# Performance work log

Hardware: AMD Instinct MI355X
Metric: run time of the kernel (lower is better)

## Reference

```python
import jax, jax.numpy as jnp
import numpy as np

E = 1024
H = 16
D = E // H  # head dim 64
B = 2
S = 2048


def setup_inputs() -> dict:
    key = jax.random.key(0)
    k1, k2, k3, k4, k5 = jax.random.split(key, 5)
    scale = 1.0 / np.sqrt(E)
    return {
        "x": jax.random.normal(k1, (B, S, E), dtype=jnp.float32),
        "W_in": jax.random.normal(k2, (E, 3 * E), dtype=jnp.float32) * scale,
        "b_in": jnp.zeros((3 * E,), dtype=jnp.float32),
        "W_out": jax.random.normal(k3, (E, E), dtype=jnp.float32) * scale,
        "b_out": jnp.zeros((E,), dtype=jnp.float32),
        "causal_mask": 1,
    }


def reference(x, W_in, b_in, W_out, b_out, causal_mask):
    b, s, e = x.shape
    qkv = x @ W_in + b_in                      # [B,S,3E]
    q, k, v = jnp.split(qkv, 3, axis=-1)
    # [B,S,E] -> [B,H,S,D]
    q = q.reshape(b, s, H, D).transpose(0, 2, 1, 3)
    k = k.reshape(b, s, H, D).transpose(0, 2, 1, 3)
    v = v.reshape(b, s, H, D).transpose(0, 2, 1, 3)
    scores = jnp.einsum("bhqd,bhkd->bhqk", q, k)
    if causal_mask:
        # mask applied before scaling in the original; -inf is scale-invariant
        mask = jnp.triu(jnp.ones((s, s), dtype=bool), k=1)
        scores = jnp.where(mask, -jnp.inf, scores)
    scores = scores / np.sqrt(D)
    weight = jax.nn.softmax(scores, axis=-1)
    out = jnp.einsum("bhqk,bhkd->bhqd", weight, v)   # [B,H,S,D]
    out = out.transpose(0, 2, 1, 3).reshape(b, s, e)
    return out @ W_out + b_out
```

## Files before the change

### kernel.cpp

```cpp
#include <hip/hip_runtime.h>
#include <hip/hip_bf16.h>
#include <cmath>

typedef __bf16 bf16;
typedef __attribute__((ext_vector_type(8))) __bf16 bf16x8;
typedef __attribute__((ext_vector_type(4))) __bf16 bf16x4;
typedef __attribute__((ext_vector_type(4))) float f32x4;
typedef __attribute__((ext_vector_type(16))) float f32x16;
typedef unsigned int u32;

constexpr int S  = 2048;
constexpr int E  = 1024;
constexpr int H  = 16;
constexpr int D  = 64;
constexpr int B  = 2;
constexpr int M  = B * S;
constexpr int N3 = 3 * E;
constexpr int NROWS = B * H * S;

static __device__ __forceinline__ void gload16(const void* g, void* l) {
  __builtin_amdgcn_global_load_lds((const __attribute__((address_space(1))) void*)g,
                                   (__attribute__((address_space(3))) void*)l, 16, 0, 0);
}

static __device__ __forceinline__ u32 pack2(float a, float b) {
  union { bf16 h[2]; u32 u; } r;
  r.h[0] = (bf16)a; r.h[1] = (bf16)b;
  return r.u;
}
typedef union { u32 w[4]; bf16x8 v; } FU;

__global__ void k_cvt(const float* __restrict__ in, bf16* __restrict__ out) {
  const int i = (blockIdx.x * blockDim.x + threadIdx.x) * 4;
  const float4 v = *(const float4*)(in + i);
  bf16x4 o = { (bf16)v.x, (bf16)v.y, (bf16)v.z, (bf16)v.w };
  *(bf16x4*)(out + i) = o;
}

__global__ void k_transpose_cvt(const float* __restrict__ in, bf16* __restrict__ out,
                                int R, int C) {
  __shared__ float t[32][33];
  const int c0 = blockIdx.x * 32, r0 = blockIdx.y * 32;
  const int tx = threadIdx.x, ty = threadIdx.y;
  #pragma unroll
  for (int j = 0; j < 32; j += 8)
    t[ty + j][tx] = in[(size_t)(r0 + ty + j) * C + c0 + tx];
  __syncthreads();
  #pragma unroll
  for (int j = 0; j < 32; j += 8)
    out[(size_t)(c0 + ty + j) * R + r0 + tx] = (bf16)t[tx][ty + j];
}

template<int EPI>
__global__ __launch_bounds__(256) void k_gemm(
    const bf16* __restrict__ A, const bf16* __restrict__ Bt,
    const float* __restrict__ bias, float* __restrict__ outF,
    bf16* __restrict__ oQ, bf16* __restrict__ oK, bf16* __restrict__ oV,
    int Kdim, int Nn)
{
  __shared__ __align__(16) char smem[65536];
  const int tid = threadIdx.x;
  const int lane = tid & 63, w = tid >> 6;
  const int lane15 = lane & 15, quad = lane >> 4;
  const int wm = w >> 1, wn = w & 1;

  const int nbx = Nn >> 7;
  const int nwg = gridDim.x;
  const int bid = blockIdx.x;
  const int swz = (bid & 7) * (nwg >> 3) + (bid >> 3);
  const int bn0 = (swz % nbx) * 128;
  const int bm0 = (swz / nbx) * 128;

  const int so0 = w * 1024 + lane * 16;
  int srow[4], slk[4];
  #pragma unroll
  for (int p = 0; p < 4; ++p) {
    const int o = p * 4096 + so0;
    const int row = o >> 7, cbyte = o & 127;
    srow[p] = row;
    slk[p] = (cbyte ^ ((row & 7) << 4)) >> 1;
  }

  f32x4 acc[4][4] = {};
  const int nkt = Kdim >> 6;

  #pragma unroll
  for (int p = 0; p < 4; ++p) {
    gload16(A  + (size_t)(bm0 + srow[p]) * Kdim + slk[p], smem +         p * 4096 + w * 1024);
    gload16(Bt + (size_t)(bn0 + srow[p]) * Kdim + slk[p], smem + 32768 + p * 4096 + w * 1024);
  }

  #pragma unroll 1
  for (int kt = 0; kt < nkt; ++kt) {
    const int cur = kt & 1;
    __builtin_amdgcn_s_barrier();
    if (kt + 1 < nkt) {
      const int k0 = (kt + 1) << 6;
      const int nb = (cur ^ 1) * 16384;
      #pragma unroll
      for (int p = 0; p < 4; ++p) {
        gload16(A  + (size_t)(bm0 + srow[p]) * Kdim + k0 + slk[p],
                smem + nb +         p * 4096 + w * 1024);
        gload16(Bt + (size_t)(bn0 + srow[p]) * Kdim + k0 + slk[p],
                smem + nb + 32768 + p * 4096 + w * 1024);
      }
      asm volatile("s_waitcnt vmcnt(8)" ::: "memory");
    } else {
      asm volatile("s_waitcnt vmcnt(0)" ::: "memory");
    }
    __builtin_amdgcn_s_barrier();

    const char* cA = smem + cur * 16384;
    const char* cB = smem + 32768 + cur * 16384;
    #pragma unroll
    for (int kk = 0; kk < 2; ++kk) {
      bf16x8 af[4], bfr[4];
      #pragma unroll
      for (int f = 0; f < 4; ++f) {
        const int ra = wm * 64 + f * 16 + lane15;
        af[f] = *(const bf16x8*)(cA + ra * 128 +
                 ((kk * 64 + (quad << 4)) ^ ((ra & 7) << 4)));
        const int rb = wn * 64 + f * 16 + lane15;
        bfr[f] = *(const bf16x8*)(cB + rb * 128 +
                 ((kk * 64 + (quad << 4)) ^ ((rb & 7) << 4)));
      }
      #pragma unroll
      for (int i = 0; i < 4; ++i)
        #pragma unroll
        for (int j = 0; j < 4; ++j)
          acc[i][j] = __builtin_amdgcn_mfma_f32_16x16x32_bf16(af[i], bfr[j], acc[i][j], 0, 0, 0);
    }
  }

  if constexpr (EPI == 1) {
    #pragma unroll
    for (int i = 0; i < 4; ++i)
      #pragma unroll
      for (int j = 0; j < 4; ++j) {
        const int n = bn0 + wn * 64 + j * 16 + lane15;
        const float bv = bias[n];
        #pragma unroll
        for (int r = 0; r < 4; ++r) {
          const int m = bm0 + wm * 64 + i * 16 + quad * 4 + r;
          outF[(size_t)m * E + n] = acc[i][j][r] + bv;
        }
      }
  } else {
    const int which = bn0 >> 10;
    const int b  = bm0 >> 11;
    const int s0 = bm0 & (S - 1);
    const int cn0 = bn0 & (E - 1);
    if (which < 2) {
      bf16* dst = (which == 0) ? oQ : oK;
      __builtin_amdgcn_s_barrier();
      char* lC = smem;
      #pragma unroll
      for (int j = 0; j < 4; ++j) {
        const int n_loc = wn * 64 + j * 16 + lane15;
        const float bv = bias[bn0 + n_loc];
        #pragma unroll
        for (int i = 0; i < 4; ++i)
          #pragma unroll
          for (int r = 0; r < 4; ++r) {
            const int m_loc = wm * 64 + i * 16 + quad * 4 + r;
            *(bf16*)(lC + m_loc * 256 + ((n_loc * 2) ^ ((m_loc & 7) << 4))) =
                (bf16)(acc[i][j][r] + bv);
          }
      }
      __builtin_amdgcn_s_barrier();
      const int h0 = cn0 >> 6;
      #pragma unroll
      for (int it = 0; it < 8; ++it) {
        const int cch = w * 64 + it * 8 + (lane >> 3);
        const int m_loc = cch >> 1, hh = cch & 1, piece = lane & 7;
        const bf16x8 vv = *(const bf16x8*)(lC + m_loc * 256 +
                          ((hh * 128 + piece * 16) ^ ((m_loc & 7) << 4)));
        *(bf16x8*)(dst + ((size_t)(b * H + h0 + hh) * S + s0 + m_loc) * D + piece * 8) = vv;
      }
    } else {
      #pragma unroll
      for (int j = 0; j < 4; ++j) {
        const int n_loc = wn * 64 + j * 16 + lane15;
        const int cn = cn0 + n_loc;
        const int h = cn >> 6, d = cn & 63;
        const float bv = bias[bn0 + n_loc];
        bf16* base = oV + ((size_t)(b * H + h) * D + d) * S + s0 + wm * 64;
        #pragma unroll
        for (int i = 0; i < 4; ++i) {
          bf16x4 pk = { (bf16)(acc[i][j][0] + bv), (bf16)(acc[i][j][1] + bv),
                        (bf16)(acc[i][j][2] + bv), (bf16)(acc[i][j][3] + bv) };
          *(bf16x4*)(base + i * 16 + quad * 4) = pk;
        }
      }
    }
  }
}

__global__ __launch_bounds__(256, 2) void k_attn(
    const bf16* __restrict__ Qb, const bf16* __restrict__ Kb, const bf16* __restrict__ Vt,
    bf16* __restrict__ pO0, bf16* __restrict__ pO1,
    float* __restrict__ pM, float* __restrict__ pL, const int* __restrict__ cmask)
{
  __shared__ __align__(16) char lK[2][64 * 128];
  __shared__ __align__(16) char lV[2][64 * 128];
  __shared__ __align__(16) float corr_lds[4][32];
  __shared__ __align__(16) float lrow_lds[4][32];

  const int tid = threadIdx.x, lane = tid & 63, w = tid >> 6;
  const int h = lane >> 5, q31 = lane & 31;
  const int bh = blockIdx.x;
  const int jb = blockIdx.y;
  const int causal = cmask[0];
  const float S2 = 0.18033688011112042f;

  const bf16* Qh = Qb + (size_t)bh * S * D;
  const bf16* Kh = Kb + (size_t)bh * S * D;
  const bf16* Vh = Vt + (size_t)bh * D * S;

  const int so0 = w * 1024 + lane * 16;
  int srow[2], slk[2];
  #pragma unroll
  for (int p = 0; p < 2; ++p) {
    const int o = p * 4096 + so0;
    const int row = o >> 7, cbv = o & 127;
    srow[p] = row;
    slk[p] = (cbv ^ ((row & 7) << 4)) >> 1;
  }
  const int swz = (q31 & 7) << 4;

  #pragma unroll 1
  for (int pidx = 0; pidx < 2; ++pidx) {
    const int c  = pidx ? (15 - jb) : jb;
    const int t0 = causal ? (pidx ? (c + 1) : 0) : (pidx ? 16 : 0);
    const int t1 = causal ? (pidx ? (2 * c + 2) : (c + 1)) : (pidx ? 32 : 16);
    const int q0w = c * 128 + 32 * w;
    const int qg  = q0w + q31;

    __builtin_amdgcn_s_barrier();

    bf16x8 qf[4];
    #pragma unroll
    for (int ds = 0; ds < 4; ++ds)
      qf[ds] = *(const bf16x8*)(Qh + (size_t)qg * D + 16 * ds + 8 * h);

    #pragma unroll
    for (int p = 0; p < 2; ++p) {
      gload16(Kh + (size_t)(t0 * 64 + srow[p]) * D + slk[p], lK[0] + p * 4096 + so0);
      gload16(Vh + (size_t)srow[p] * S + t0 * 64 + slk[p],   lV[0] + p * 4096 + so0);
    }

    f32x16 o0 = {}, o1 = {};
    float mrun = -INFINITY, lr = 0.f;

    #pragma unroll 1
    for (int t = t0; t < t1; ++t) {
      const int cb = (t - t0) & 1;
      __builtin_amdgcn_s_barrier();
      if (t + 1 < t1) {
        const int kb = (t + 1) * 64;
        #pragma unroll
        for (int p = 0; p < 2; ++p) {
          gload16(Kh + (size_t)(kb + srow[p]) * D + slk[p], lK[cb ^ 1] + p * 4096 + so0);
          gload16(Vh + (size_t)srow[p] * S + kb + slk[p],   lV[cb ^ 1] + p * 4096 + so0);
        }
        asm volatile("s_waitcnt vmcnt(4)" ::: "memory");
      } else {
        asm volatile("s_waitcnt vmcnt(0)" ::: "memory");
      }
      __builtin_amdgcn_s_barrier();

      const bool active = !causal || (64 * t <= q0w + 31);
      if (active) {
        f32x16 s0v = {}, s1v = {};
        __builtin_amdgcn_s_setprio(1);
        #pragma unroll
        for (int ds = 0; ds < 4; ++ds) {
          const int col = (32 * ds + 16 * h) ^ swz;
          const bf16x8 kf0 = *(const bf16x8*)(lK[cb] + q31 * 128 + col);
          const bf16x8 kf1 = *(const bf16x8*)(lK[cb] + (32 + q31) * 128 + col);
          s0v = __builtin_amdgcn_mfma_f32_32x32x16_bf16(kf0, qf[ds], s0v, 0, 0, 0);
          s1v = __builtin_amdgcn_mfma_f32_32x32x16_bf16(kf1, qf[ds], s1v, 0, 0, 0);
        }
        __builtin_amdgcn_s_setprio(0);

        if (causal && (64 * t + 63 > q0w)) {
          #pragma unroll
          for (int r = 0; r < 16; ++r) {
            const int kg = 64 * t + (r & 3) + 8 * (r >> 2) + 4 * h;
            if (kg > qg)      s0v[r] = -INFINITY;
            if (kg + 32 > qg) s1v[r] = -INFINITY;
          }
        }

        float a8[8];
        #pragma unroll
        for (int i = 0; i < 8; ++i)
          a8[i] = fmaxf(fmaxf(s0v[i], s0v[i + 8]), fmaxf(s1v[i], s1v[i + 8]));
        float tmax = fmaxf(fmaxf(fmaxf(a8[0], a8[1]), fmaxf(a8[2], a8[3])),
                           fmaxf(fmaxf(a8[4], a8[5]), fmaxf(a8[6], a8[7])));
        tmax = fmaxf(tmax, __shfl_xor(tmax, 32, 64));

        const bool nogrow = __all(tmax <= mrun);
        const float mnew = nogrow ? mrun : fmaxf(mrun, tmax);
        float corrf = 1.f;
        if (!nogrow) {
          corrf = __builtin_amdgcn_exp2f((mrun - mnew) * S2);
          corr_lds[w][q31] = corrf;
        }
        const float msc = mnew * S2;

        #pragma unroll
        for (int r = 0; r < 16; ++r) {
          s0v[r] = __builtin_amdgcn_exp2f(__builtin_fmaf(s0v[r], S2, -msc));
          s1v[r] = __builtin_amdgcn_exp2f(__builtin_fmaf(s1v[r], S2, -msc));
        }

        float b8[8];
        #pragma unroll
        for (int i = 0; i < 8; ++i)
          b8[i] = (s0v[i] + s0v[i + 8]) + (s1v[i] + s1v[i + 8]);
        float psum = ((b8[0] + b8[1]) + (b8[2] + b8[3])) + ((b8[4] + b8[5]) + (b8[6] + b8[7]));
        psum += __shfl_xor(psum, 32, 64);
        lr = lr * corrf + psum;
        mrun = mnew;

        u32 pk[8][2];
        #pragma unroll
        for (int jj = 0; jj < 4; ++jj) {
          pk[jj][0]     = pack2(s0v[4 * jj],     s0v[4 * jj + 1]);
          pk[jj][1]     = pack2(s0v[4 * jj + 2], s0v[4 * jj + 3]);
          pk[jj + 4][0] = pack2(s1v[4 * jj],     s1v[4 * jj + 1]);
          pk[jj + 4][1] = pack2(s1v[4 * jj + 2], s1v[4 * jj + 3]);
        }

        if (!nogrow) {
          #pragma unroll
          for (int j = 0; j < 4; ++j) {
            const f32x4 cv = *(const f32x4*)&corr_lds[w][8 * j + 4 * h];
            #pragma unroll
            for (int sr = 0; sr < 4; ++sr) {
              o0[4 * j + sr] *= cv[sr];
              o1[4 * j + sr] *= cv[sr];
            }
          }
        }

        __builtin_amdgcn_s_setprio(1);
        #pragma unroll
        for (int ks = 0; ks < 4; ++ks) {
          u32 a0 = pk[2 * ks][0], b0 = pk[2 * ks + 1][0];
          u32 a1 = pk[2 * ks][1], b1 = pk[2 * ks + 1][1];
          asm volatile("v_permlane32_swap_b32 %0, %1" : "+v"(a0), "+v"(b0));
          asm volatile("v_permlane32_swap_b32 %0, %1" : "+v"(a1), "+v"(b1));
          FU f; f.w[0] = a0; f.w[1] = a1; f.w[2] = b0; f.w[3] = b1;
          const int col = (32 * ks + 16 * h) ^ swz;
          const bf16x8 vf0 = *(const bf16x8*)(lV[cb] + q31 * 128 + col);
          const bf16x8 vf1 = *(const bf16x8*)(lV[cb] + (32 + q31) * 128 + col);
          o0 = __builtin_amdgcn_mfma_f32_32x32x16_bf16(f.v, vf0, o0, 0, 0, 0);
          o1 = __builtin_amdgcn_mfma_f32_32x32x16_bf16(f.v, vf1, o1, 0, 0, 0);
        }
        __builtin_amdgcn_s_setprio(0);
      }
    }

    if (h == 0) {
      pM[(size_t)pidx * NROWS + bh * S + qg] = mrun;
      pL[(size_t)pidx * NROWS + bh * S + qg] = lr;
    }
    lrow_lds[w][q31] = lr;
    bf16* po = pidx ? pO1 : pO0;
    #pragma unroll
    for (int j = 0; j < 4; ++j) {
      const f32x4 lv = *(const f32x4*)&lrow_lds[w][8 * j + 4 * h];
      #pragma unroll
      for (int sr = 0; sr < 4; ++sr) {
        const int r = 4 * j + sr;
        const float inv = lv[sr] > 0.f ? 1.0f / lv[sr] : 0.f;
        const int qrow = q0w + (r & 3) + 8 * (r >> 2) + 4 * h;
        bf16* dst = po + ((size_t)(bh * S + qrow)) * D;
        dst[q31]      = (bf16)(o0[r] * inv);
        dst[32 + q31] = (bf16)(o1[r] * inv);
      }
    }
  }
}

__global__ __launch_bounds__(256) void k_combine(
    const bf16* __restrict__ pO0, const bf16* __restrict__ pO1,
    const float* __restrict__ pM, const float* __restrict__ pL,
    bf16* __restrict__ AO)
{
  const float S2 = 0.18033688011112042f;
  const int idx = blockIdx.x * 256 + threadIdx.x;
  const int row = idx >> 3, d0 = (idx & 7) * 8;
  const float mA = pM[row], mB = pM[NROWS + row];
  const float lA = pL[row], lB = pL[NROWS + row];
  const float m = fmaxf(mA, mB);
  const float wA = lA > 0.f ? lA * __builtin_amdgcn_exp2f((mA - m) * S2) : 0.f;
  const float wB = lB > 0.f ? lB * __builtin_amdgcn_exp2f((mB - m) * S2) : 0.f;
  const float inv = 1.0f / (wA + wB);
  const bf16x8 a = *(const bf16x8*)(pO0 + (size_t)row * D + d0);
  const bf16x8 b = *(const bf16x8*)(pO1 + (size_t)row * D + d0);
  bf16x8 o;
  #pragma unroll
  for (int i = 0; i < 8; ++i)
    o[i] = (bf16)((wA * (float)a[i] + wB * (float)b[i]) * inv);
  const int bb = row >> 15, hh = (row >> 11) & 15, s = row & 2047;
  *(bf16x8*)(AO + ((size_t)(bb * S + s)) * E + hh * D + d0) = o;
}

extern "C" void kernel_launch(void* const* d_in, const int* in_sizes, int n_in,
                              void* d_out, int out_size, void* d_ws, size_t ws_size,
                              hipStream_t stream) {
  (void)in_sizes; (void)n_in; (void)out_size; (void)ws_size;
  const float* x     = (const float*)d_in[0];
  const float* W_in  = (const float*)d_in[1];
  const float* b_in  = (const float*)d_in[2];
  const float* W_out = (const float*)d_in[3];
  const float* b_out = (const float*)d_in[4];
  const int*   cmask = (const int*)d_in[5];

  char* ws = (char*)d_ws;
  bf16* xb    = (bf16*)ws; ws += (size_t)M * E * 2;
  bf16* wtin  = (bf16*)ws; ws += (size_t)N3 * E * 2;
  bf16* wtout = (bf16*)ws; ws += (size_t)E * E * 2;
  bf16* qB    = (bf16*)ws; ws += (size_t)B * H * S * D * 2;
  bf16* kB    = (bf16*)ws; ws += (size_t)B * H * S * D * 2;
  bf16* vT    = (bf16*)ws; ws += (size_t)B * H * S * D * 2;
  bf16* ao    = (bf16*)ws; ws += (size_t)M * E * 2;
  bf16* pO1   = (bf16*)ws; ws += (size_t)NROWS * D * 2;
  float* pMb  = (float*)ws; ws += (size_t)2 * NROWS * 4;
  float* pLb  = (float*)ws; ws += (size_t)2 * NROWS * 4;
  bf16* pO0   = xb;

  k_cvt<<<M * E / 1024, 256, 0, stream>>>(x, xb);
  k_transpose_cvt<<<dim3(N3 / 32, E / 32), dim3(32, 8), 0, stream>>>(W_in, wtin, E, N3);
  k_transpose_cvt<<<dim3(E / 32, E / 32), dim3(32, 8), 0, stream>>>(W_out, wtout, E, E);
  k_gemm<0><<<dim3((M / 128) * (N3 / 128)), 256, 0, stream>>>(
      xb, wtin, b_in, nullptr, qB, kB, vT, E, N3);
  k_attn<<<dim3(32, 16), 256, 0, stream>>>(qB, kB, vT, pO0, pO1, pMb, pLb, cmask);
  k_combine<<<NROWS * 8 / 256, 256, 0, stream>>>(pO0, pO1, pMb, pLb, ao);
  k_gemm<1><<<dim3((M / 128) * (E / 128)), 256, 0, stream>>>(
      ao, wtout, b_out, (float*)d_out, nullptr, nullptr, nullptr, E, E);
}
```

Measured before the change: 115.0 us.

## Store K/V in MFMA-fragment order and load attention operands directly from global

The QKV GEMM epilogue now writes K and V in a tiled layout that matches the MFMA operand fragments. The attention kernel can then load K and V straight from global memory into registers with coalesced 16-byte loads, and drops the LDS double buffering and the per-tile barriers. Each wave also stops its loop at its own causal bound instead of idling through masked tiles. The trade-off is that every wave issues its own global/L2 reads of K/V tiles with no explicit prefetch, so load latency is exposed unless the cache hits and other waves hide it.

```diff
diff --git a/kernel.cpp b/kernel.cpp
--- a/kernel.cpp
+++ b/kernel.cpp
@@ -151,7 +151,6 @@
     const int s0 = bm0 & (S - 1);
     const int cn0 = bn0 & (E - 1);
     if (which < 2) {
-      bf16* dst = (which == 0) ? oQ : oK;
       __builtin_amdgcn_s_barrier();
       char* lC = smem;
       #pragma unroll
@@ -175,21 +174,34 @@
         const int m_loc = cch >> 1, hh = cch & 1, piece = lane & 7;
         const bf16x8 vv = *(const bf16x8*)(lC + m_loc * 256 +
                           ((hh * 128 + piece * 16) ^ ((m_loc & 7) << 4)));
-        *(bf16x8*)(dst + ((size_t)(b * H + h0 + hh) * S + s0 + m_loc) * D + piece * 8) = vv;
+        if (which == 0) {
+          *(bf16x8*)(oQ + ((size_t)(b * H + h0 + hh) * S + s0 + m_loc) * D + piece * 8) = vv;
+        } else {
+          const size_t hb = (size_t)(b * H + h0 + hh) * S * D;
+          const int tile = (s0 + m_loc) >> 6;
+          const int row = m_loc & 63;
+          *(bf16x8*)(oK + hb + (size_t)tile * 4096 + (piece >> 1) * 1024 +
+                     (row >> 5) * 512 + (32 * (piece & 1) + (row & 31)) * 8) = vv;
+        }
       }
     } else {
       #pragma unroll
       for (int j = 0; j < 4; ++j) {
         const int n_loc = wn * 64 + j * 16 + lane15;
         const int cn = cn0 + n_loc;
-        const int h = cn >> 6, d = cn & 63;
+        const int hv = cn >> 6, dd = cn & 63;
         const float bv = bias[bn0 + n_loc];
-        bf16* base = oV + ((size_t)(b * H + h) * D + d) * S + s0 + wm * 64;
+        const size_t hb = (size_t)(b * H + hv) * S * D;
         #pragma unroll
         for (int i = 0; i < 4; ++i) {
+          const int scol_g = s0 + wm * 64 + i * 16 + quad * 4;
+          const int vtile = scol_g >> 6;
+          const int cg = (scol_g & 63) >> 3;
           bf16x4 pk = { (bf16)(acc[i][j][0] + bv), (bf16)(acc[i][j][1] + bv),
                         (bf16)(acc[i][j][2] + bv), (bf16)(acc[i][j][3] + bv) };
-          *(bf16x4*)(base + i * 16 + quad * 4) = pk;
+          *(bf16x4*)(oV + hb + (size_t)vtile * 4096 + (cg >> 1) * 1024 +
+                     (dd >> 5) * 512 + (32 * (cg & 1) + (dd & 31)) * 8 +
+                     (quad & 1) * 4) = pk;
         }
       }
     }
@@ -197,14 +209,12 @@
 }
 
 __global__ __launch_bounds__(256, 2) void k_attn(
-    const bf16* __restrict__ Qb, const bf16* __restrict__ Kb, const bf16* __restrict__ Vt,
+    const bf16* __restrict__ Qb, const bf16* __restrict__ Kf, const bf16* __restrict__ Vf,
     bf16* __restrict__ pO0, bf16* __restrict__ pO1,
     float* __restrict__ pM, float* __restrict__ pL, const int* __restrict__ cmask)
 {
-  __shared__ __align__(16) char lK[2][64 * 128];
-  __shared__ __align__(16) char lV[2][64 * 128];
-  __shared__ __align__(16) float corr_lds[4][32];
-  __shared__ __align__(16) float lrow_lds[4][32];
+  __shared__ float corr_lds[4][32];
+  __shared__ float lrow_lds[4][32];
 
   const int tid = threadIdx.x, lane = tid & 63, w = tid >> 6;
   const int h = lane >> 5, q31 = lane & 31;
@@ -214,19 +224,8 @@
   const float S2 = 0.18033688011112042f;
 
   const bf16* Qh = Qb + (size_t)bh * S * D;
-  const bf16* Kh = Kb + (size_t)bh * S * D;
-  const bf16* Vh = Vt + (size_t)bh * D * S;
-
-  const int so0 = w * 1024 + lane * 16;
-  int srow[2], slk[2];
-  #pragma unroll
-  for (int p = 0; p < 2; ++p) {
-    const int o = p * 4096 + so0;
-    const int row = o >> 7, cbv = o & 127;
-    srow[p] = row;
-    slk[p] = (cbv ^ ((row & 7) << 4)) >> 1;
-  }
-  const int swz = (q31 & 7) << 4;
+  const bf16* Kh = Kf + (size_t)bh * S * D;
+  const bf16* Vh = Vf + (size_t)bh * S * D;
 
   #pragma unroll 1
   for (int pidx = 0; pidx < 2; ++pidx) {
@@ -235,132 +234,113 @@
     const int t1 = causal ? (pidx ? (2 * c + 2) : (c + 1)) : (pidx ? 32 : 16);
     const int q0w = c * 128 + 32 * w;
     const int qg  = q0w + q31;
-
-    __builtin_amdgcn_s_barrier();
+    const int t1w = causal ? min(t1, (q0w + 31) / 64 + 1) : t1;
 
     bf16x8 qf[4];
     #pragma unroll
     for (int ds = 0; ds < 4; ++ds)
       qf[ds] = *(const bf16x8*)(Qh + (size_t)qg * D + 16 * ds + 8 * h);
 
-    #pragma unroll
-    for (int p = 0; p < 2; ++p) {
-      gload16(Kh + (size_t)(t0 * 64 + srow[p]) * D + slk[p], lK[0] + p * 4096 + so0);
-      gload16(Vh + (size_t)srow[p] * S + t0 * 64 + slk[p],   lV[0] + p * 4096 + so0);
-    }
-
     f32x16 o0 = {}, o1 = {};
     float mrun = -INFINITY, lr = 0.f;
 
     #pragma unroll 1
-    for (int t = t0; t < t1; ++t) {
-      const int cb = (t - t0) & 1;
-      __builtin_amdgcn_s_barrier();
-      if (t + 1 < t1) {
-        const int kb = (t + 1) * 64;
-        #pragma unroll
-        for (int p = 0; p < 2; ++p) {
-          gload16(Kh + (size_t)(kb + srow[p]) * D + slk[p], lK[cb ^ 1] + p * 4096 + so0);
-          gload16(Vh + (size_t)srow[p] * S + kb + slk[p],   lV[cb ^ 1] + p * 4096 + so0);
+    for (int t = t0; t < t1w; ++t) {
+      const bf16* ktb = Kh + (size_t)t * 4096;
+      const bf16* vtb = Vh + (size_t)t * 4096;
+
+      bf16x8 kf0[4], kf1[4];
+      #pragma unroll
+      for (int ds = 0; ds < 4; ++ds) {
+        kf0[ds] = *(const bf16x8*)(ktb + ds * 1024 +       lane * 8);
+        kf1[ds] = *(const bf16x8*)(ktb + ds * 1024 + 512 + lane * 8);
+      }
+
+      f32x16 s0v = {}, s1v = {};
+      __builtin_amdgcn_s_setprio(1);
+      #pragma unroll
+      for (int ds = 0; ds < 4; ++ds) {
+        s0v = __builtin_amdgcn_mfma_f32_32x32x16_bf16(kf0[ds], qf[ds], s0v, 0, 0, 0);
+        s1v = __builtin_amdgcn_mfma_f32_32x32x16_bf16(kf1[ds], qf[ds], s1v, 0, 0, 0);
+      }
+      __builtin_amdgcn_s_setprio(0);
+
+      if (causal && (64 * t + 63 > q0w)) {
+        #pragma unroll
+        for (int r = 0; r < 16; ++r) {
+          const int kg = 64 * t + (r & 3) + 8 * (r >> 2) + 4 * h;
+          if (kg > qg)      s0v[r] = -INFINITY;
+          if (kg + 32 > qg) s1v[r] = -INFINITY;
         }
-        asm volatile("s_waitcnt vmcnt(4)" ::: "memory");
-      } else {
-        asm volatile("s_waitcnt vmcnt(0)" ::: "memory");
-      }
-      __builtin_amdgcn_s_barrier();
-
-      const bool active = !causal || (64 * t <= q0w + 31);
-      if (active) {
-        f32x16 s0v = {}, s1v = {};
-        __builtin_amdgcn_s_setprio(1);
-        #pragma unroll
-        for (int ds = 0; ds < 4; ++ds) {
-          const int col = (32 * ds + 16 * h) ^ swz;
-          const bf16x8 kf0 = *(const bf16x8*)(lK[cb] + q31 * 128 + col);
-          const bf16x8 kf1 = *(const bf16x8*)(lK[cb] + (32 + q31) * 128 + col);
-          s0v = __builtin_amdgcn_mfma_f32_32x32x16_bf16(kf0, qf[ds], s0v, 0, 0, 0);
-          s1v = __builtin_amdgcn_mfma_f32_32x32x16_bf16(kf1, qf[ds], s1v, 0, 0, 0);
-        }
-        __builtin_amdgcn_s_setprio(0);
-
-        if (causal && (64 * t + 63 > q0w)) {
+      }
+
+      float a8[8];
+      #pragma unroll
+      for (int i = 0; i < 8; ++i)
+        a8[i] = fmaxf(fmaxf(s0v[i], s0v[i + 8]), fmaxf(s1v[i], s1v[i + 8]));
+      float tmax = fmaxf(fmaxf(fmaxf(a8[0], a8[1]), fmaxf(a8[2], a8[3])),
+                         fmaxf(fmaxf(a8[4], a8[5]), fmaxf(a8[6], a8[7])));
+      tmax = fmaxf(tmax, __shfl_xor(tmax, 32, 64));
+
+      const bool nogrow = __all(tmax <= mrun);
+      const float mnew = nogrow ? mrun : fmaxf(mrun, tmax);
+      float corrf = 1.f;
+      if (!nogrow) {
+        corrf = __builtin_amdgcn_exp2f((mrun - mnew) * S2);
+        corr_lds[w][q31] = corrf;
+      }
+      const float msc = mnew * S2;
+
+      #pragma unroll
+      for (int r = 0; r < 16; ++r) {
+        s0v[r] = __builtin_amdgcn_exp2f(__builtin_fmaf(s0v[r], S2, -msc));
+        s1v[r] = __builtin_amdgcn_exp2f(__builtin_fmaf(s1v[r], S2, -msc));
+      }
+
+      float b8[8];
+      #pragma unroll
+      for (int i = 0; i < 8; ++i)
+        b8[i] = (s0v[i] + s0v[i + 8]) + (s1v[i] + s1v[i + 8]);
+      float psum = ((b8[0] + b8[1]) + (b8[2] + b8[3])) + ((b8[4] + b8[5]) + (b8[6] + b8[7]));
+      psum += __shfl_xor(psum, 32, 64);
+      lr = lr * corrf + psum;
+      mrun = mnew;
+
+      u32 pk[8][2];
+      #pragma unroll
+      for (int jj = 0; jj < 4; ++jj) {
+        pk[jj][0]     = pack2(s0v[4 * jj],     s0v[4 * jj + 1]);
+        pk[jj][1]     = pack2(s0v[4 * jj + 2], s0v[4 * jj + 3]);
+        pk[jj + 4][0] = pack2(s1v[4 * jj],     s1v[4 * jj + 1]);
+        pk[jj + 4][1] = pack2(s1v[4 * jj + 2], s1v[4 * jj + 3]);
+      }
+
+      if (!nogrow) {
+        #pragma unroll
+        for (int j = 0; j < 4; ++j) {
+          const f32x4 cv = *(const f32x4*)&corr_lds[w][8 * j + 4 * h];
           #pragma unroll
-          for (int r = 0; r < 16; ++r) {
-            const int kg = 64 * t + (r & 3) + 8 * (r >> 2) + 4 * h;
-            if (kg > qg)      s0v[r] = -INFINITY;
-            if (kg + 32 > qg) s1v[r] = -INFINITY;
+          for (int sr = 0; sr < 4; ++sr) {
+            o0[4 * j + sr] *= cv[sr];
+            o1[4 * j + sr] *= cv[sr];
           }
         }
-
-        float a8[8];
-        #pragma unroll
-        for (int i = 0; i < 8; ++i)
-          a8[i] = fmaxf(fmaxf(s0v[i], s0v[i + 8]), fmaxf(s1v[i], s1v[i + 8]));
-        float tmax = fmaxf(fmaxf(fmaxf(a8[0], a8[1]), fmaxf(a8[2], a8[3])),
-                           fmaxf(fmaxf(a8[4], a8[5]), fmaxf(a8[6], a8[7])));
-        tmax = fmaxf(tmax, __shfl_xor(tmax, 32, 64));
-
-        const bool nogrow = __all(tmax <= mrun);
-        const float mnew = nogrow ? mrun : fmaxf(mrun, tmax);
-        float corrf = 1.f;
-        if (!nogrow) {
-          corrf = __builtin_amdgcn_exp2f((mrun - mnew) * S2);
-          corr_lds[w][q31] = corrf;
-        }
-        const float msc = mnew * S2;
-
-        #pragma unroll
-        for (int r = 0; r < 16; ++r) {
-          s0v[r] = __builtin_amdgcn_exp2f(__builtin_fmaf(s0v[r], S2, -msc));
-          s1v[r] = __builtin_amdgcn_exp2f(__builtin_fmaf(s1v[r], S2, -msc));
-        }
-
-        float b8[8];
-        #pragma unroll
-        for (int i = 0; i < 8; ++i)
-          b8[i] = (s0v[i] + s0v[i + 8]) + (s1v[i] + s1v[i + 8]);
-        float psum = ((b8[0] + b8[1]) + (b8[2] + b8[3])) + ((b8[4] + b8[5]) + (b8[6] + b8[7]));
-        psum += __shfl_xor(psum, 32, 64);
-        lr = lr * corrf + psum;
-        mrun = mnew;
-
-        u32 pk[8][2];
-        #pragma unroll
-        for (int jj = 0; jj < 4; ++jj) {
-          pk[jj][0]     = pack2(s0v[4 * jj],     s0v[4 * jj + 1]);
-          pk[jj][1]     = pack2(s0v[4 * jj + 2], s0v[4 * jj + 3]);
-          pk[jj + 4][0] = pack2(s1v[4 * jj],     s1v[4 * jj + 1]);
-          pk[jj + 4][1] = pack2(s1v[4 * jj + 2], s1v[4 * jj + 3]);
-        }
-
-        if (!nogrow) {
-          #pragma unroll
-          for (int j = 0; j < 4; ++j) {
-            const f32x4 cv = *(const f32x4*)&corr_lds[w][8 * j + 4 * h];
-            #pragma unroll
-            for (int sr = 0; sr < 4; ++sr) {
-              o0[4 * j + sr] *= cv[sr];
-              o1[4 * j + sr] *= cv[sr];
-            }
-          }
-        }
-
-        __builtin_amdgcn_s_setprio(1);
-        #pragma unroll
-        for (int ks = 0; ks < 4; ++ks) {
-          u32 a0 = pk[2 * ks][0], b0 = pk[2 * ks + 1][0];
-          u32 a1 = pk[2 * ks][1], b1 = pk[2 * ks + 1][1];
-          asm volatile("v_permlane32_swap_b32 %0, %1" : "+v"(a0), "+v"(b0));
-          asm volatile("v_permlane32_swap_b32 %0, %1" : "+v"(a1), "+v"(b1));
-          FU f; f.w[0] = a0; f.w[1] = a1; f.w[2] = b0; f.w[3] = b1;
-          const int col = (32 * ks + 16 * h) ^ swz;
-          const bf16x8 vf0 = *(const bf16x8*)(lV[cb] + q31 * 128 + col);
-          const bf16x8 vf1 = *(const bf16x8*)(lV[cb] + (32 + q31) * 128 + col);
-          o0 = __builtin_amdgcn_mfma_f32_32x32x16_bf16(f.v, vf0, o0, 0, 0, 0);
-          o1 = __builtin_amdgcn_mfma_f32_32x32x16_bf16(f.v, vf1, o1, 0, 0, 0);
-        }
-        __builtin_amdgcn_s_setprio(0);
-      }
+      }
+
+      __builtin_amdgcn_s_setprio(1);
+      #pragma unroll
+      for (int ks = 0; ks < 4; ++ks) {
+        u32 a0 = pk[2 * ks][0], b0 = pk[2 * ks + 1][0];
+        u32 a1 = pk[2 * ks][1], b1 = pk[2 * ks + 1][1];
+        asm volatile("v_permlane32_swap_b32 %0, %1" : "+v"(a0), "+v"(b0));
+        asm volatile("v_permlane32_swap_b32 %0, %1" : "+v"(a1), "+v"(b1));
+        FU f; f.w[0] = a0; f.w[1] = a1; f.w[2] = b0; f.w[3] = b1;
+        const bf16x8 vf0 = *(const bf16x8*)(vtb + ks * 1024 +       lane * 8);
+        const bf16x8 vf1 = *(const bf16x8*)(vtb + ks * 1024 + 512 + lane * 8);
+        o0 = __builtin_amdgcn_mfma_f32_32x32x16_bf16(f.v, vf0, o0, 0, 0, 0);
+        o1 = __builtin_amdgcn_mfma_f32_32x32x16_bf16(f.v, vf1, o1, 0, 0, 0);
+      }
+      __builtin_amdgcn_s_setprio(0);
     }
 
     if (h == 0) {
@@ -425,8 +405,8 @@
   bf16* wtin  = (bf16*)ws; ws += (size_t)N3 * E * 2;
   bf16* wtout = (bf16*)ws; ws += (size_t)E * E * 2;
   bf16* qB    = (bf16*)ws; ws += (size_t)B * H * S * D * 2;
-  bf16* kB    = (bf16*)ws; ws += (size_t)B * H * S * D * 2;
-  bf16* vT    = (bf16*)ws; ws += (size_t)B * H * S * D * 2;
+  bf16* kF    = (bf16*)ws; ws += (size_t)B * H * S * D * 2;
+  bf16* vF    = (bf16*)ws; ws += (size_t)B * H * S * D * 2;
   bf16* ao    = (bf16*)ws; ws += (size_t)M * E * 2;
   bf16* pO1   = (bf16*)ws; ws += (size_t)NROWS * D * 2;
   float* pMb  = (float*)ws; ws += (size_t)2 * NROWS * 4;
@@ -437,8 +417,8 @@
   k_transpose_cvt<<<dim3(N3 / 32, E / 32), dim3(32, 8), 0, stream>>>(W_in, wtin, E, N3);
   k_transpose_cvt<<<dim3(E / 32, E / 32), dim3(32, 8), 0, stream>>>(W_out, wtout, E, E);
   k_gemm<0><<<dim3((M / 128) * (N3 / 128)), 256, 0, stream>>>(
-      xb, wtin, b_in, nullptr, qB, kB, vT, E, N3);
-  k_attn<<<dim3(32, 16), 256, 0, stream>>>(qB, kB, vT, pO0, pO1, pMb, pLb, cmask);
+      xb, wtin, b_in, nullptr, qB, kF, vF, E, N3);
+  k_attn<<<dim3(32, 16), 256, 0, stream>>>(qB, kF, vF, pO0, pO1, pMb, pLb, cmask);
   k_combine<<<NROWS * 8 / 256, 256, 0, stream>>>(pO0, pO1, pMb, pLb, ao);
   k_gemm<1><<<dim3((M / 128) * (E / 128)), 256, 0, stream>>>(
       ao, wtout, b_out, (float*)d_out, nullptr, nullptr, nullptr, E, E);
```

After: 117.0 us. Within noise of the previous version (+1.7%).
